# Optimization experiments

Measured on AMD Instinct MI355X. Metric: run time of the kernel, lower is better.

## Reference

```python
import jax, jax.numpy as jnp
import numpy as np

T, D, H, E, TOP_K = 4096, 512, 2048, 16, 2


def setup_inputs() -> dict:
    key = jax.random.key(0)
    ks = jax.random.split(key, 4)
    x = jax.random.normal(ks[0], (T, D), dtype=jnp.float32)
    Wg = jax.random.normal(ks[1], (D, E), dtype=jnp.float32) * 0.02
    bg = jnp.zeros((E,), dtype=jnp.float32)
    W1 = jax.random.normal(ks[2], (E, D, H), dtype=jnp.float32) * 0.02
    b1 = jnp.zeros((E, H), dtype=jnp.float32)
    W2 = jax.random.normal(ks[3], (E, H, D), dtype=jnp.float32) * 0.02
    b2 = jnp.zeros((E, D), dtype=jnp.float32)
    return {"x": x, "Wg": Wg, "bg": bg, "W1": W1, "b1": b1, "W2": W2, "b2": b2}


def reference(x, Wg, bg, W1, b1, W2, b2):
    # NaiveGate: linear -> top-k -> softmax over the k selected logits
    logits = x @ Wg + bg                               # [T, E]
    gate_vals, gate_idx = jax.lax.top_k(logits, TOP_K)  # [T, k]
    gate_score = jax.nn.softmax(gate_vals, axis=-1)     # returned by gate; NOT applied to output (faithful to source)

    # combine weights: how many top-k slots of each token map to each expert
    counts = jax.nn.one_hot(gate_idx, E, dtype=x.dtype).sum(axis=1)  # [T, E]

    # Expert FFN (grouped GEMM expressed densely over the fixed expert axis)
    h = jax.nn.gelu(jnp.einsum('td,edh->eth', x, W1) + b1[:, None, :])  # [E, T, H]
    y = jnp.einsum('eth,ehd->etd', h, W2) + b2[:, None, :]              # [E, T, D]

    # Combine: unweighted sum over the token's top-k experts (matches .sum(dim=1) in source)
    out = jnp.einsum('etd,te->td', y, counts)                            # [T, D]
    return out, gate_idx, gate_score
```

## Files before the change

### kernel.cpp

```cpp
#include <hip/hip_runtime.h>
#include <math.h>

#define T_ 4096
#define D_ 512
#define H_ 2048
#define E_ 16
#define RCAP 10240

typedef short bf16x8 __attribute__((ext_vector_type(8)));
typedef float f32x4 __attribute__((ext_vector_type(4)));

__device__ __forceinline__ unsigned short f2bf(float f) {
  union { float f; unsigned u; } v; v.f = f;
  unsigned r = v.u + 0x7fffu + ((v.u >> 16) & 1u);
  return (unsigned short)(r >> 16);
}
__device__ __forceinline__ float bf2f(unsigned short u) {
  union { unsigned u; float f; } v; v.u = ((unsigned)u) << 16;
  return v.f;
}

__global__ void gate_kernel(const float* __restrict__ x,
                            const float* __restrict__ Wg,
                            const float* __restrict__ bg,
                            float* __restrict__ out,
                            int* __restrict__ tok2e) {
  const int lane = threadIdx.x & 63;
  const int t = blockIdx.x * 4 + (threadIdx.x >> 6);
  const int e = lane & 15, q = lane >> 4;
  const float4* x4 = (const float4*)(x + (size_t)t * D_ + q * 128);
  float acc = 0.f;
#pragma unroll 4
  for (int i = 0; i < 32; ++i) {
    float4 v = x4[i];
    const float* wp = Wg + (q * 128 + i * 4) * E_ + e;
    acc += v.x * wp[0];
    acc += v.y * wp[E_];
    acc += v.z * wp[2 * E_];
    acc += v.w * wp[3 * E_];
  }
  acc += __shfl_xor(acc, 16);
  acc += __shfl_xor(acc, 32);
  const float logit = acc + bg[e];
  float v1 = logit; int i1 = e;
#pragma unroll
  for (int s = 1; s < 16; s <<= 1) {
    float ov = __shfl_xor(v1, s); int oi = __shfl_xor(i1, s);
    if (ov > v1 || (ov == v1 && oi < i1)) { v1 = ov; i1 = oi; }
  }
  float v2 = (e == i1) ? -INFINITY : logit; int i2 = e;
#pragma unroll
  for (int s = 1; s < 16; s <<= 1) {
    float ov = __shfl_xor(v2, s); int oi = __shfl_xor(i2, s);
    if (ov > v2 || (ov == v2 && oi < i2)) { v2 = ov; i2 = oi; }
  }
  if (lane == 0) {
    const float ed = __expf(v2 - v1);
    const float inv = 1.f / (1.f + ed);
    const size_t gidx = (size_t)T_ * D_;
    out[gidx + t * 2]     = (float)i1;
    out[gidx + t * 2 + 1] = (float)i2;
    out[gidx + T_ * 2 + t * 2]     = inv;
    out[gidx + T_ * 2 + t * 2 + 1] = ed * inv;
    tok2e[t * 2] = i1; tok2e[t * 2 + 1] = i2;
  }
}

__global__ void count_kernel(const int* __restrict__ tok2e,
                             int* __restrict__ cnt2,
                             int* __restrict__ offs, int* __restrict__ tileoff,
                             int* __restrict__ rowbuf) {
  __shared__ int h[E_];
  if (threadIdx.x < E_) h[threadIdx.x] = 0;
  __syncthreads();
  for (int i = threadIdx.x; i < 2 * T_; i += 256) atomicAdd(&h[tok2e[i]], 1);
  __syncthreads();
  if (threadIdx.x == 0) {
    int o = 0, to = 0;
    offs[0] = 0; tileoff[0] = 0;
    for (int e = 0; e < E_; ++e) {
      int mt = (h[e] + 127) >> 7;
      o += mt << 7; to += mt;
      offs[e + 1] = o; tileoff[e + 1] = to;
    }
  }
  for (int i = threadIdx.x; i < E_ * 16; i += 256) cnt2[i] = 0;
  for (int i = threadIdx.x; i < RCAP; i += 256) rowbuf[i] = -1;
}

__global__ void scatter_kernel(const int* __restrict__ tok2e, int* __restrict__ cnt2,
                               const int* __restrict__ offs, int* __restrict__ rowbuf,
                               int* __restrict__ tok2row) {
  const int t = blockIdx.x * blockDim.x + threadIdx.x;
#pragma unroll
  for (int k = 0; k < 2; ++k) {
    int e = tok2e[t * 2 + k];
    int slot = atomicAdd(&cnt2[e * 16], 1);
    int row = offs[e] + slot;
    rowbuf[row] = t;
    tok2row[t * 2 + k] = row;
  }
}

__global__ void gather_kernel(const float* __restrict__ x,
                              const int* __restrict__ rowbuf,
                              const int* __restrict__ offs,
                              unsigned short* __restrict__ xg) {
  const int row = blockIdx.x;
  if (row >= offs[16]) return;
  const int t = rowbuf[row];
  const int lane = threadIdx.x;
  float4 a = make_float4(0.f, 0.f, 0.f, 0.f), b = a;
  if (t >= 0) {
    const float4* p = (const float4*)(x + (size_t)t * D_ + lane * 8);
    a = p[0]; b = p[1];
  }
  unsigned w0 = f2bf(a.x) | (f2bf(a.y) << 16);
  unsigned w1 = f2bf(a.z) | (f2bf(a.w) << 16);
  unsigned w2 = f2bf(b.x) | (f2bf(b.y) << 16);
  unsigned w3 = f2bf(b.z) | (f2bf(b.w) << 16);
  *(uint4*)(xg + (size_t)row * D_ + lane * 8) = make_uint4(w0, w1, w2, w3);
}

template <int K, int N>
__global__ __launch_bounds__(256) void wtrans_kernel(const float* __restrict__ src,
                                                     unsigned short* __restrict__ dst) {
  __shared__ unsigned short tile[64][72];
  const int e = blockIdx.z;
  const int n0 = blockIdx.x << 6, k0 = blockIdx.y << 6;
  const int tid = threadIdx.x;
  const int tr = tid >> 4, tc = (tid & 15) << 2;
  const float* s = src + ((size_t)e * K + k0) * N + n0;
#pragma unroll
  for (int p = 0; p < 4; ++p) {
    float4 v = *(const float4*)(s + (size_t)(tr + p * 16) * N + tc);
    tile[tc + 0][tr + p * 16] = f2bf(v.x);
    tile[tc + 1][tr + p * 16] = f2bf(v.y);
    tile[tc + 2][tr + p * 16] = f2bf(v.z);
    tile[tc + 3][tr + p * 16] = f2bf(v.w);
  }
  __syncthreads();
  const int wr = tid >> 2, wc = (tid & 3) << 4;
  unsigned short* d = dst + ((size_t)e * N + n0 + wr) * K + k0 + wc;
  *(uint4*)d       = *(const uint4*)&tile[wr][wc];
  *(uint4*)(d + 8) = *(const uint4*)&tile[wr][wc + 8];
}

template <int KDIM, int NTOT, int NTILE, bool GELU>
__global__ __launch_bounds__(256) void ffn_gemm(
    const unsigned short* __restrict__ A_g, const unsigned short* __restrict__ Bt_g,
    const float* __restrict__ bias_g, unsigned short* __restrict__ out_g,
    const int* __restrict__ offs, const int* __restrict__ tileoff) {
  constexpr int JN = NTILE / 32;
  __shared__ unsigned short As[128][72];
  __shared__ unsigned short Bs[NTILE][72];
  const int mt = blockIdx.x;
  if (mt >= tileoff[16]) return;
  int e = 0;
  while (tileoff[e + 1] <= mt) ++e;
  const int row0 = offs[e] + ((mt - tileoff[e]) << 7);
  const int n0 = blockIdx.y * NTILE;
  const int tid = threadIdx.x;
  const int lane = tid & 63;
  const int m_off = ((tid >> 6) & 1) << 6;
  const int n_off = (tid >> 7) * (NTILE / 2);

  f32x4 acc[4][JN];
#pragma unroll
  for (int i = 0; i < 4; ++i)
#pragma unroll
    for (int j = 0; j < JN; ++j) acc[i][j] = (f32x4){0.f, 0.f, 0.f, 0.f};

  const int arow = tid >> 1, ahalf = tid & 1;
  const unsigned short* Aptr = A_g + (size_t)(row0 + arow) * KDIM + ahalf * 32;
  int brow, bcol;
  if (NTILE == 128) { brow = tid >> 1; bcol = (tid & 1) * 32; }
  else              { brow = tid >> 2; bcol = (tid & 3) * 16; }
  const unsigned short* Bptr = Bt_g + ((size_t)e * NTOT + n0 + brow) * KDIM + bcol;

  for (int k0 = 0; k0 < KDIM; k0 += 64) {
    const uint4* asrc = (const uint4*)(Aptr + k0);
    uint4 a0 = asrc[0], a1 = asrc[1], a2 = asrc[2], a3 = asrc[3];
    const uint4* bsrc = (const uint4*)(Bptr + k0);
    uint4 b0 = bsrc[0], b1 = bsrc[1], b2, b3;
    if (NTILE == 128) { b2 = bsrc[2]; b3 = bsrc[3]; }
    uint4* adst = (uint4*)&As[arow][ahalf * 32];
    adst[0] = a0; adst[1] = a1; adst[2] = a2; adst[3] = a3;
    if (NTILE == 128) {
      uint4* bdst = (uint4*)&Bs[brow][bcol];
      bdst[0] = b0; bdst[1] = b1; bdst[2] = b2; bdst[3] = b3;
    } else {
      uint4* bdst = (uint4*)&Bs[brow][bcol];
      bdst[0] = b0; bdst[1] = b1;
    }
    __syncthreads();
#pragma unroll
    for (int kk = 0; kk < 64; kk += 32) {
      const int kidx = kk + ((lane >> 4) << 3);
      bf16x8 af[4], bfr[JN];
#pragma unroll
      for (int i = 0; i < 4; ++i)
        af[i] = *(const bf16x8*)&As[m_off + i * 16 + (lane & 15)][kidx];
#pragma unroll
      for (int j = 0; j < JN; ++j)
        bfr[j] = *(const bf16x8*)&Bs[n_off + j * 16 + (lane & 15)][kidx];
#pragma unroll
      for (int i = 0; i < 4; ++i)
#pragma unroll
        for (int j = 0; j < JN; ++j)
          acc[i][j] = __builtin_amdgcn_mfma_f32_16x16x32_bf16(af[i], bfr[j], acc[i][j], 0, 0, 0);
    }
    __syncthreads();
  }
  const float* bias = bias_g + (size_t)e * NTOT;
  const int quad = lane >> 4, lcol = lane & 15;
#pragma unroll
  for (int j = 0; j < JN; ++j) {
    const int col = n0 + n_off + j * 16 + lcol;
    const float bv = bias[col];
#pragma unroll
    for (int i = 0; i < 4; ++i) {
      const int rbase = row0 + m_off + i * 16 + (quad << 2);
      f32x4 v = acc[i][j];
#pragma unroll
      for (int r = 0; r < 4; ++r) {
        float y = v[r] + bv;
        if (GELU) y = 0.5f * y * (1.f + erff(y * 0.70710678118f));
        out_g[(size_t)(rbase + r) * NTOT + col] = f2bf(y);
      }
    }
  }
}

__global__ void combine_kernel(const unsigned short* __restrict__ ybuf,
                               const int* __restrict__ tok2row,
                               float* __restrict__ out) {
  const int t = blockIdx.x, lane = threadIdx.x;
  const int rA = tok2row[t * 2], rB = tok2row[t * 2 + 1];
  const uint4 va = *(const uint4*)(ybuf + (size_t)rA * D_ + lane * 8);
  const uint4 vb = *(const uint4*)(ybuf + (size_t)rB * D_ + lane * 8);
  const unsigned short* pa = (const unsigned short*)&va;
  const unsigned short* pb = (const unsigned short*)&vb;
  float o[8];
#pragma unroll
  for (int i = 0; i < 8; ++i) o[i] = bf2f(pa[i]) + bf2f(pb[i]);
  float4* po = (float4*)(out + (size_t)t * D_ + lane * 8);
  po[0] = make_float4(o[0], o[1], o[2], o[3]);
  po[1] = make_float4(o[4], o[5], o[6], o[7]);
}

extern "C" void kernel_launch(void* const* d_in, const int* in_sizes, int n_in,
                              void* d_out, int out_size, void* d_ws, size_t ws_size,
                              hipStream_t stream) {
  const float* x  = (const float*)d_in[0];
  const float* Wg = (const float*)d_in[1];
  const float* bg = (const float*)d_in[2];
  const float* W1 = (const float*)d_in[3];
  const float* b1 = (const float*)d_in[4];
  const float* W2 = (const float*)d_in[5];
  const float* b2 = (const float*)d_in[6];
  float* out = (float*)d_out;
  char* ws = (char*)d_ws;

  int* cnt2    = (int*)(ws);
  int* offs    = (int*)(ws + 2048);
  int* tileoff = (int*)(ws + 3072);
  int* tok2e   = (int*)(ws + 4096);
  int* tok2row = (int*)(ws + 4096 + 32768);
  int* rowbuf  = (int*)(ws + 4096 + 65536);
  unsigned short* xg   = (unsigned short*)(ws + (1 << 20));
  unsigned short* ybuf = xg;
  unsigned short* hbuf = (unsigned short*)(ws + (size_t)(12 << 20));
  unsigned short* Wt   = (unsigned short*)(ws + (size_t)(52 << 20));

  gate_kernel<<<T_ / 4, 256, 0, stream>>>(x, Wg, bg, out, tok2e);
  count_kernel<<<1, 256, 0, stream>>>(tok2e, cnt2, offs, tileoff, rowbuf);
  scatter_kernel<<<T_ / 256, 256, 0, stream>>>(tok2e, cnt2, offs, rowbuf, tok2row);
  gather_kernel<<<RCAP, 64, 0, stream>>>(x, rowbuf, offs, xg);
  wtrans_kernel<D_, H_><<<dim3(H_ / 64, D_ / 64, E_), 256, 0, stream>>>(W1, Wt);
  ffn_gemm<512, 2048, 128, true><<<dim3(80, 16), 256, 0, stream>>>(xg, Wt, b1, hbuf, offs, tileoff);
  wtrans_kernel<H_, D_><<<dim3(D_ / 64, H_ / 64, E_), 256, 0, stream>>>(W2, Wt);
  ffn_gemm<2048, 512, 64, false><<<dim3(80, 8), 256, 0, stream>>>(hbuf, Wt, b2, ybuf, offs, tileoff);
  combine_kernel<<<T_, 64, 0, stream>>>(ybuf, tok2row, out);
}
```

Measured before the change: 315.5 us.

## Use direct global-to-LDS loads with XOR-swizzled tiles in FFN GEMM; stage gate weights in LDS

```diff
diff --git a/kernel.cpp b/kernel.cpp
--- a/kernel.cpp
+++ b/kernel.cpp
@@ -19,12 +19,20 @@
   union { unsigned u; float f; } v; v.u = ((unsigned)u) << 16;
   return v.f;
 }
-
-__global__ void gate_kernel(const float* __restrict__ x,
-                            const float* __restrict__ Wg,
-                            const float* __restrict__ bg,
-                            float* __restrict__ out,
-                            int* __restrict__ tok2e) {
+__device__ __forceinline__ void gload_lds16(const unsigned short* g, unsigned short* l) {
+  __builtin_amdgcn_global_load_lds((const __attribute__((address_space(1))) void*)g,
+                                   (__attribute__((address_space(3))) void*)l, 16, 0, 0);
+}
+
+__global__ __launch_bounds__(256) void gate_kernel(const float* __restrict__ x,
+                                                   const float* __restrict__ Wg,
+                                                   const float* __restrict__ bg,
+                                                   float* __restrict__ out,
+                                                   int* __restrict__ tok2e) {
+  __shared__ float wgl[D_ * E_];
+  for (int i = threadIdx.x; i < D_ * E_ / 4; i += 256)
+    *(float4*)&wgl[i * 4] = ((const float4*)Wg)[i];
+  __syncthreads();
   const int lane = threadIdx.x & 63;
   const int t = blockIdx.x * 4 + (threadIdx.x >> 6);
   const int e = lane & 15, q = lane >> 4;
@@ -33,7 +41,7 @@
 #pragma unroll 4
   for (int i = 0; i < 32; ++i) {
     float4 v = x4[i];
-    const float* wp = Wg + (q * 128 + i * 4) * E_ + e;
+    const float* wp = &wgl[(q * 128 + i * 4) * E_ + e];
     acc += v.x * wp[0];
     acc += v.y * wp[E_];
     acc += v.z * wp[2 * E_];
@@ -152,8 +160,9 @@
     const float* __restrict__ bias_g, unsigned short* __restrict__ out_g,
     const int* __restrict__ offs, const int* __restrict__ tileoff) {
   constexpr int JN = NTILE / 32;
-  __shared__ unsigned short As[128][72];
-  __shared__ unsigned short Bs[NTILE][72];
+  constexpr int BRPW = NTILE / 4;
+  __shared__ unsigned short As[128 * 64];
+  __shared__ unsigned short Bs[NTILE * 64];
   const int mt = blockIdx.x;
   if (mt >= tileoff[16]) return;
   int e = 0;
@@ -162,7 +171,8 @@
   const int n0 = blockIdx.y * NTILE;
   const int tid = threadIdx.x;
   const int lane = tid & 63;
-  const int m_off = ((tid >> 6) & 1) << 6;
+  const int w = tid >> 6;
+  const int m_off = (w & 1) << 6;
   const int n_off = (tid >> 7) * (NTILE / 2);
 
   f32x4 acc[4][JN];
@@ -171,39 +181,38 @@
 #pragma unroll
     for (int j = 0; j < JN; ++j) acc[i][j] = (f32x4){0.f, 0.f, 0.f, 0.f};
 
-  const int arow = tid >> 1, ahalf = tid & 1;
-  const unsigned short* Aptr = A_g + (size_t)(row0 + arow) * KDIM + ahalf * 32;
-  int brow, bcol;
-  if (NTILE == 128) { brow = tid >> 1; bcol = (tid & 1) * 32; }
-  else              { brow = tid >> 2; bcol = (tid & 3) * 16; }
-  const unsigned short* Bptr = Bt_g + ((size_t)e * NTOT + n0 + brow) * KDIM + bcol;
+  const int r_in = lane >> 3;
+  const int cbg = (lane & 7) ^ r_in;
+  const unsigned short* gA = A_g + (size_t)(row0 + w * 32 + r_in) * KDIM + cbg * 8;
+  const unsigned short* gB = Bt_g + ((size_t)e * NTOT + n0 + w * BRPW + r_in) * KDIM + cbg * 8;
+  unsigned short* lA = &As[w * 32 * 64];
+  unsigned short* lB = &Bs[w * BRPW * 64];
+
+  const int q = lane >> 4, fr = lane & 15;
 
   for (int k0 = 0; k0 < KDIM; k0 += 64) {
-    const uint4* asrc = (const uint4*)(Aptr + k0);
-    uint4 a0 = asrc[0], a1 = asrc[1], a2 = asrc[2], a3 = asrc[3];
-    const uint4* bsrc = (const uint4*)(Bptr + k0);
-    uint4 b0 = bsrc[0], b1 = bsrc[1], b2, b3;
-    if (NTILE == 128) { b2 = bsrc[2]; b3 = bsrc[3]; }
-    uint4* adst = (uint4*)&As[arow][ahalf * 32];
-    adst[0] = a0; adst[1] = a1; adst[2] = a2; adst[3] = a3;
-    if (NTILE == 128) {
-      uint4* bdst = (uint4*)&Bs[brow][bcol];
-      bdst[0] = b0; bdst[1] = b1; bdst[2] = b2; bdst[3] = b3;
-    } else {
-      uint4* bdst = (uint4*)&Bs[brow][bcol];
-      bdst[0] = b0; bdst[1] = b1;
-    }
+#pragma unroll
+    for (int j = 0; j < 4; ++j)
+      gload_lds16(gA + (size_t)j * 8 * KDIM + k0, lA + j * 8 * 64);
+#pragma unroll
+    for (int j = 0; j < BRPW / 8; ++j)
+      gload_lds16(gB + (size_t)j * 8 * KDIM + k0, lB + j * 8 * 64);
     __syncthreads();
 #pragma unroll
     for (int kk = 0; kk < 64; kk += 32) {
-      const int kidx = kk + ((lane >> 4) << 3);
       bf16x8 af[4], bfr[JN];
 #pragma unroll
-      for (int i = 0; i < 4; ++i)
-        af[i] = *(const bf16x8*)&As[m_off + i * 16 + (lane & 15)][kidx];
-#pragma unroll
-      for (int j = 0; j < JN; ++j)
-        bfr[j] = *(const bf16x8*)&Bs[n_off + j * 16 + (lane & 15)][kidx];
+      for (int i = 0; i < 4; ++i) {
+        const int r = m_off + i * 16 + fr;
+        const int sw = ((((kk >> 3) + q) ^ (r & 7)) << 3);
+        af[i] = *(const bf16x8*)&As[r * 64 + sw];
+      }
+#pragma unroll
+      for (int j = 0; j < JN; ++j) {
+        const int r = n_off + j * 16 + fr;
+        const int sw = ((((kk >> 3) + q) ^ (r & 7)) << 3);
+        bfr[j] = *(const bf16x8*)&Bs[r * 64 + sw];
+      }
 #pragma unroll
       for (int i = 0; i < 4; ++i)
 #pragma unroll
@@ -213,14 +222,13 @@
     __syncthreads();
   }
   const float* bias = bias_g + (size_t)e * NTOT;
-  const int quad = lane >> 4, lcol = lane & 15;
 #pragma unroll
   for (int j = 0; j < JN; ++j) {
-    const int col = n0 + n_off + j * 16 + lcol;
+    const int col = n0 + n_off + j * 16 + fr;
     const float bv = bias[col];
 #pragma unroll
     for (int i = 0; i < 4; ++i) {
-      const int rbase = row0 + m_off + i * 16 + (quad << 2);
+      const int rbase = row0 + m_off + i * 16 + (q << 2);
       f32x4 v = acc[i][j];
 #pragma unroll
       for (int r = 0; r < 4; ++r) {
```

After: 294.2 us. 6.8% less time.
